# Kernel optimization log

Hardware: AMD Instinct MI355X
Metric: run time of the kernel (lower is better)

Reference implementation:

```python
import jax, jax.numpy as jnp
import numpy as np

DIM = 128
DIM_HEAD = 32
HEADS = DIM // DIM_HEAD
W1, W2, W3 = 7, 7, 7


def _rel_pos_indices():
    # matches the torch buffer construction
    g = np.stack(np.meshgrid(np.arange(W1), np.arange(W2), np.arange(W3), indexing='ij'))
    grid = g.reshape(3, -1).T  # (n, 3)
    rel = grid[:, None, :] - grid[None, :, :]
    rel[..., 0] += W1 - 1
    rel[..., 1] += W2 - 1
    rel[..., 2] += W3 - 1
    strides = np.array([(2 * W2 - 1) * (2 * W3 - 1), 2 * W3 - 1, 1])
    return (rel * strides).sum(-1).astype(np.int32)  # (n, n)


def setup_inputs() -> dict:
    key = jax.random.key(0)
    k1, k2, k3, k4 = jax.random.split(key, 4)
    x = jax.random.normal(k1, (1, 8, 8, 8, W1, W2, W3, DIM), dtype=jnp.float32)
    w_qkv = jax.random.normal(k2, (DIM, 3 * DIM), dtype=jnp.float32) * (DIM ** -0.5)
    w_out = jax.random.normal(k3, (DIM, DIM), dtype=jnp.float32) * (DIM ** -0.5)
    n_rel = (2 * W1 - 1) * (2 * W2 - 1) * (2 * W3 - 1)  # 2197
    bias_table = jax.random.normal(k4, (n_rel, HEADS), dtype=jnp.float32) * 0.02
    rel_idx = jnp.asarray(_rel_pos_indices())
    return {"x": x, "w_qkv": w_qkv, "w_out": w_out, "bias_table": bias_table, "rel_idx": rel_idx}


def reference(x, w_qkv, w_out, bias_table, rel_idx):
    b, X, Y, Z, w1, w2, w3, d = x.shape
    n = w1 * w2 * w3
    scale = DIM_HEAD ** -0.5
    xr = x.reshape(-1, n, d)                           # (B, n, d), B = b*X*Y*Z
    qkv = xr @ w_qkv                                    # (B, n, 3d)
    q, k, v = jnp.split(qkv, 3, axis=-1)
    def heads(t):
        B = t.shape[0]
        return t.reshape(B, n, HEADS, DIM_HEAD).transpose(0, 2, 1, 3)  # (B, h, n, dh)
    q, k, v = heads(q) * scale, heads(k), heads(v)
    sim = jnp.einsum('bhid,bhjd->bhij', q, k)           # (B, h, n, n)
    bias = bias_table[rel_idx]                          # (n, n, h)
    sim = sim + bias.transpose(2, 0, 1)[None]
    attn = jax.nn.softmax(sim, axis=-1)
    out = jnp.einsum('bhij,bhjd->bhid', attn, v)        # (B, h, n, dh)
    out = out.transpose(0, 2, 1, 3).reshape(-1, n, d)   # (B, n, d)
    out = out @ w_out
    return out.reshape(b, X, Y, Z, w1, w2, w3, d)
```

## Files before the change

kernel.cpp:

```cpp
#include <hip/hip_runtime.h>

#define N 343
#define NP 352
#define DIM 128
#define HEADS 4
#define DH 32

typedef float  f32x16 __attribute__((ext_vector_type(16)));
typedef float  float4v __attribute__((ext_vector_type(4)));
typedef short  short8 __attribute__((ext_vector_type(8)));
typedef unsigned uint4v __attribute__((ext_vector_type(4)));
typedef unsigned uint2v __attribute__((ext_vector_type(2)));

#define MFMA __builtin_amdgcn_mfma_f32_32x32x16_bf16

static __device__ __forceinline__ unsigned cvtpk_bf16(float lo, float hi) {
  unsigned r;
  asm("v_cvt_pk_bf16_f32 %0, %1, %2" : "=v"(r) : "v"(lo), "v"(hi));
  return r;
}
static __device__ __forceinline__ void swap32(unsigned &a, unsigned &b) {
  asm("v_permlane32_swap_b32 %0, %1" : "+v"(a), "+v"(b));
}
static __device__ __forceinline__ float exp2v(float x) {
  float r;
  asm("v_exp_f32 %0, %1" : "=v"(r) : "v"(x));
  return r;
}
static __device__ __forceinline__ float max3v(float a, float b, float c) {
  float r;
  asm("v_max3_f32 %0, %1, %2, %3" : "=v"(r) : "v"(a), "v"(b), "v"(c));
  return r;
}
static __device__ __forceinline__ unsigned short bf16u(float a) {
  unsigned u = __builtin_bit_cast(unsigned, a);
  unsigned r = u + 0x7fffu + ((u >> 16) & 1u);
  return (unsigned short)(r >> 16);
}

__global__ __launch_bounds__(256) void bias_kernel(
    const float* __restrict__ table, const int* __restrict__ rel,
    float* __restrict__ prep) {
  int row = blockIdx.x * 256 + threadIdx.x;
  if (row >= HEADS * 11 * 2 * NP) return;
  int i = row % NP;
  int t = row / NP;
  int half = t & 1;
  int tj = t >> 1;
  int jt = tj % 11;
  int h = tj / 11;
  float* dst = prep + (size_t)row * 16;
#pragma unroll
  for (int r = 0; r < 16; ++r) {
    int j = jt * 32 + (r & 3) + ((r >> 2) << 3) + (half << 2);
    float v;
    if (j >= N) v = -1.44e30f;
    else if (i >= N) v = 0.f;
    else v = table[rel[i * N + j] * HEADS + h] * 1.4426950408889634f;
    dst[r] = v;
  }
}

static __device__ __forceinline__ void attend(
    int i0, uint4v qAu, uint4v qBu,
    const unsigned short* __restrict__ Kb, const unsigned short* __restrict__ Vt,
    const float* __restrict__ bp, float* __restrict__ outw,
    int l31, int half, int swz) {
  short8 q0 = __builtin_bit_cast(short8, qAu);
  short8 q1 = __builtin_bit_cast(short8, qBu);
  const float* bpi = bp + (size_t)(i0 + l31) * 16;

  f32x16 O;
#pragma unroll
  for (int r = 0; r < 16; ++r) O[r] = 0.f;
  float m_run = -3.0e38f, l_run = 0.f;

  f32x16 Tn = *(const f32x16*)(bpi);
  for (int jt = 0; jt < 11; ++jt) {
    f32x16 T = Tn;
    if (jt < 10) Tn = *(const f32x16*)(bpi + (size_t)(jt + 1) * 11264);

    const int krow = (jt * 32 + l31) * 40;
    short8 ka0 = *(const short8*)&Kb[krow + ((half * 8) ^ swz)];
    short8 ka1 = *(const short8*)&Kb[krow + ((half * 8 + 16) ^ swz)];
    T = MFMA(ka0, q0, T, 0, 0, 0);
    T = MFMA(ka1, q1, T, 0, 0, 0);

    float g0 = max3v(T[0],  T[1],  T[2]);
    float g1 = max3v(T[3],  T[4],  T[5]);
    float g2 = max3v(T[6],  T[7],  T[8]);
    float g3 = max3v(T[9],  T[10], T[11]);
    float g4 = max3v(T[12], T[13], T[14]);
    float h0 = max3v(g0, g1, g2);
    float h1 = max3v(g3, g4, T[15]);
    float pm = fmaxf(h0, h1);
    pm = fmaxf(pm, __shfl_xor(pm, 32, 64));

    if (__any(pm > m_run + 11.5f)) {
      float nm = fmaxf(m_run, pm);
      float f = exp2v(m_run - nm);
      l_run *= f;
      m_run = nm;
#pragma unroll
      for (int r = 0; r < 16; ++r) {
        int iD = (r & 3) + ((r >> 2) << 3) + (half << 2);
        O[r] *= __shfl(f, iD, 64);
      }
    }

    float p[16];
#pragma unroll
    for (int r = 0; r < 16; ++r) p[r] = exp2v(T[r] - m_run);
    float s0 = (p[0] + p[1]) + (p[2] + p[3]);
    float s1 = (p[4] + p[5]) + (p[6] + p[7]);
    float s2 = (p[8] + p[9]) + (p[10] + p[11]);
    float s3 = (p[12] + p[13]) + (p[14] + p[15]);
    float ps = (s0 + s1) + (s2 + s3);
    l_run += ps + __shfl_xor(ps, 32, 64);

    unsigned k0 = cvtpk_bf16(p[0], p[1]),   k1 = cvtpk_bf16(p[2], p[3]);
    unsigned k2 = cvtpk_bf16(p[4], p[5]),   k3 = cvtpk_bf16(p[6], p[7]);
    unsigned k4 = cvtpk_bf16(p[8], p[9]),   k5 = cvtpk_bf16(p[10], p[11]);
    unsigned k6 = cvtpk_bf16(p[12], p[13]), k7 = cvtpk_bf16(p[14], p[15]);
    swap32(k0, k2); swap32(k1, k3); swap32(k4, k6); swap32(k5, k7);
    uint4v u1 = {k0, k1, k2, k3};
    uint4v u2 = {k4, k5, k6, k7};
    short8 pa1 = __builtin_bit_cast(short8, u1);
    short8 pa2 = __builtin_bit_cast(short8, u2);

    const int vrow = l31 * 360 + jt * 32;
    short8 vb1 = *(const short8*)&Vt[vrow + ((half * 8) ^ swz)];
    short8 vb2 = *(const short8*)&Vt[vrow + ((half * 8 + 16) ^ swz)];
    O = MFMA(pa1, vb1, O, 0, 0, 0);
    O = MFMA(pa2, vb2, O, 0, 0, 0);
  }

  float inv = 1.0f / l_run;
#pragma unroll
  for (int r = 0; r < 16; ++r) {
    int iD = (r & 3) + ((r >> 2) << 3) + (half << 2);
    float invr = __shfl(inv, iD, 64);
    int i = i0 + iD;
    if (i < N) outw[(size_t)i * DIM + l31] = O[r] * invr;
  }
}

__global__ __launch_bounds__(768, 3) void attn_kernel(
    const float* __restrict__ x, const float* __restrict__ wqkv,
    const float* __restrict__ prep, float* __restrict__ out) {
  const int b = blockIdx.x;
  const int sw = (b & 7) * ((int)gridDim.x >> 3) + (b >> 3);
  const int h = sw & 3;
  const int w = sw >> 2;
  const int tid = threadIdx.x;
  const int lane = tid & 63;
  const int wv = tid >> 6;
  const int l31 = lane & 31;
  const int half = lane >> 5;

  __shared__ __align__(16) unsigned short lds[29952];
  unsigned short* Xb0 = lds;
  unsigned short* Xb1 = lds + 8448;
  unsigned short* Wf  = lds + 16896;
  unsigned short* Kb = lds;
  unsigned short* Vt = lds + 14080;

  const float* xw = x + (size_t)w * (N * DIM);
  const int xsw = ((l31 >> 3) & 1) << 3;
  const bool act = (wv < 11);

  const int xrow0 = tid >> 2,  xg0 = (tid & 3) << 2;
  const int idx1  = tid + 768;
  const int xrow1 = idx1 >> 2, xg1 = (idx1 & 3) << 2;
  const bool hasx1 = (idx1 < 1408);
  const int xgs0 = xg0 ^ (((xrow0 >> 3) & 1) << 3);
  const int xgs1 = xg1 ^ (((xrow1 >> 3) & 1) << 3);

  float4v xr0v = {0.f, 0.f, 0.f, 0.f}, xr1v = {0.f, 0.f, 0.f, 0.f};

#define LOAD_STAGE(kc_)                                                     \
  {                                                                         \
    xr0v = *(const float4v*)(xw + xrow0 * DIM + (kc_) * 16 + xg0);          \
    xr1v[0] = 0.f; xr1v[1] = 0.f; xr1v[2] = 0.f; xr1v[3] = 0.f;             \
    if (hasx1 && xrow1 < N)                                                 \
      xr1v = *(const float4v*)(xw + xrow1 * DIM + (kc_) * 16 + xg1);        \
  }

#define WRITE_STAGE(XB_)                                                    \
  {                                                                         \
    unsigned h0_, h1_;                                                      \
    h0_ = cvtpk_bf16(xr0v[0], xr0v[1]);                                     \
    h1_ = cvtpk_bf16(xr0v[2], xr0v[3]);                                     \
    uint2v hv_ = {h0_, h1_};                                                \
    *(uint2v*)&(XB_)[xrow0 * 24 + xgs0] = hv_;                              \
    if (hasx1) {                                                            \
      h0_ = cvtpk_bf16(xr1v[0], xr1v[1]);                                   \
      h1_ = cvtpk_bf16(xr1v[2], xr1v[3]);                                   \
      uint2v hv2_ = {h0_, h1_};                                             \
      *(uint2v*)&(XB_)[xrow1 * 24 + xgs1] = hv2_;                           \
    }                                                                       \
  }

  f32x16 aQ, aK, aV;
#pragma unroll
  for (int r = 0; r < 16; ++r) { aQ[r] = 0.f; aK[r] = 0.f; aV[r] = 0.f; }

  LOAD_STAGE(0);
#pragma unroll
  for (int p = 0; p < 4; ++p) {
    int idx = tid + p * 768;
    int c = idx % 96, kg = (idx / 96) << 2;
    int col = ((c >> 5) << 7) + h * DH + (c & 31);
    const float* wp = wqkv + (size_t)kg * 384 + col;
#pragma unroll
    for (int u = 0; u < 4; ++u)
      Wf[c * 136 + kg + u] = bf16u(wp[(size_t)u * 384]);
  }

  for (int kc = 0; kc < 8; ++kc) {
    unsigned short* cur = (kc & 1) ? Xb1 : Xb0;
    WRITE_STAGE(cur);
    if (kc < 7) LOAD_STAGE(kc + 1);
    __syncthreads();

    if (act) {
      const int fo = (half * 8) ^ xsw;
      const int wfo = kc * 16 + half * 8;
      short8 xh = *(const short8*)&cur[(wv * 32 + l31) * 24 + fo];
      {
        short8 wh8 = *(const short8*)&Wf[l31 * 136 + wfo];
        aQ = MFMA(wh8, xh, aQ, 0, 0, 0);
      }
      {
        short8 wh8 = *(const short8*)&Wf[(32 + l31) * 136 + wfo];
        aK = MFMA(xh, wh8, aK, 0, 0, 0);
      }
      {
        short8 wh8 = *(const short8*)&Wf[(64 + l31) * 136 + wfo];
        aV = MFMA(xh, wh8, aV, 0, 0, 0);
      }
    }
  }

  __syncthreads();

  const float QS = 0.17677669529663687f * 1.4426950408889634f;
  uint4v qA = {0, 0, 0, 0}, qB = {0, 0, 0, 0};
  const int swz = ((l31 >> 3) & 3) << 3;
  if (act) {
    unsigned g0 = cvtpk_bf16(aQ[0] * QS, aQ[1] * QS);
    unsigned g1 = cvtpk_bf16(aQ[2] * QS, aQ[3] * QS);
    unsigned g2 = cvtpk_bf16(aQ[4] * QS, aQ[5] * QS);
    unsigned g3 = cvtpk_bf16(aQ[6] * QS, aQ[7] * QS);
    unsigned g4 = cvtpk_bf16(aQ[8] * QS, aQ[9] * QS);
    unsigned g5 = cvtpk_bf16(aQ[10] * QS, aQ[11] * QS);
    unsigned g6 = cvtpk_bf16(aQ[12] * QS, aQ[13] * QS);
    unsigned g7 = cvtpk_bf16(aQ[14] * QS, aQ[15] * QS);
    swap32(g0, g2); swap32(g1, g3); swap32(g4, g6); swap32(g5, g7);
    qA[0] = g0; qA[1] = g1; qA[2] = g2; qA[3] = g3;
    qB[0] = g4; qB[1] = g5; qB[2] = g6; qB[3] = g7;

#pragma unroll
    for (int r = 0; r < 16; ++r) {
      int iD = (r & 3) + ((r >> 2) << 3) + (half << 2);
      int cs = l31 ^ ((r >> 2) << 3);
      Kb[(wv * 32 + iD) * 40 + cs] = bf16u(aK[r]);
    }
#pragma unroll
    for (int r = 0; r < 16; r += 2) {
      int j0 = (r & 3) + ((r >> 2) << 3) + (half << 2);
      *(unsigned*)&Vt[l31 * 360 + wv * 32 + (j0 ^ swz)] =
          cvtpk_bf16(aV[r], aV[r + 1]);
    }
  }
  __syncthreads();

  if (act) {
    const float* bp = prep + ((size_t)(h * 22 + half) * NP) * 16;
    float* outw = out + (size_t)w * N * DIM + h * DH;
    attend(wv * 32, qA, qB, Kb, Vt, bp, outw, l31, half, swz);
  }
}

__global__ __launch_bounds__(768, 3) void proj_kernel(
    const float* __restrict__ wout, float* __restrict__ out) {
  const int w = blockIdx.x;
  const int tid = threadIdx.x;
  const int lane = tid & 63, wv = tid >> 6, l31 = lane & 31, half = lane >> 5;
  __shared__ __align__(16) unsigned short lds[19200];
  unsigned short* Oh = lds;
  unsigned short* W2h = lds + 14080;
  float* ow = out + (size_t)w * N * DIM;
  const int swz = ((l31 >> 3) & 3) << 3;
  const bool act = (wv < 11);

  f32x16 acc[4];
#pragma unroll
  for (int s = 0; s < 4; ++s)
#pragma unroll
    for (int r = 0; r < 16; ++r) acc[s][r] = 0.f;

  for (int kc = 0; kc < 4; ++kc) {
    __syncthreads();
#pragma unroll
    for (int p = 0; p < 4; ++p) {
      int idx = tid + p * 768;
      if (idx < 2816) {
        int row = idx >> 3, g = (idx & 7) << 2;
        float4v v = {0.f, 0.f, 0.f, 0.f};
        if (row < N) v = *(const float4v*)(ow + row * DIM + kc * 32 + g);
        unsigned h0 = cvtpk_bf16(v[0], v[1]);
        unsigned h1 = cvtpk_bf16(v[2], v[3]);
        uint2v hv = {h0, h1};
        int gs = g ^ (((row >> 3) & 3) << 3);
        *(uint2v*)&Oh[row * 40 + gs] = hv;
      }
    }
#pragma unroll
    for (int p = 0; p < 2; ++p) {
      int idx = tid + p * 768;
      if (idx < 1024) {
        int k = idx >> 5, n4 = (idx & 31) << 2;
        float4v v = *(const float4v*)(wout + (size_t)(kc * 32 + k) * DIM + n4);
#pragma unroll
        for (int u = 0; u < 4; ++u) {
          int n = n4 + u;
          int ks = k ^ (((n >> 3) & 3) << 3);
          W2h[n * 40 + ks] = bf16u(v[u]);
        }
      }
    }
    __syncthreads();
    if (act) {
#pragma unroll
      for (int kk = 0; kk < 2; ++kk) {
        int ro = (kk * 16 + half * 8) ^ swz;
        int rb = (wv * 32 + l31) * 40 + ro;
        short8 ah = *(const short8*)&Oh[rb];
#pragma unroll
        for (int s = 0; s < 4; ++s) {
          short8 bh = *(const short8*)&W2h[(s * 32 + l31) * 40 + ro];
          acc[s] = MFMA(ah, bh, acc[s], 0, 0, 0);
        }
      }
    }
  }
  if (act) {
#pragma unroll
    for (int s = 0; s < 4; ++s) {
#pragma unroll
      for (int r = 0; r < 16; ++r) {
        int iD = (r & 3) + ((r >> 2) << 3) + (half << 2);
        int i = wv * 32 + iD;
        if (i < N) ow[(size_t)i * DIM + s * 32 + l31] = acc[s][r];
      }
    }
  }
}

extern "C" void kernel_launch(void* const* d_in, const int* in_sizes, int n_in,
                              void* d_out, int out_size, void* d_ws, size_t ws_size,
                              hipStream_t stream) {
  const float* x     = (const float*)d_in[0];
  const float* wqkv  = (const float*)d_in[1];
  const float* wout  = (const float*)d_in[2];
  const float* table = (const float*)d_in[3];
  const int*   rel   = (const int*)d_in[4];
  float* out  = (float*)d_out;
  float* prep = (float*)d_ws;

  const int B = in_sizes[0] / (N * DIM);
  const int rows = HEADS * 11 * 2 * NP;

  bias_kernel<<<(rows + 255) / 256, 256, 0, stream>>>(table, rel, prep);
  attn_kernel<<<HEADS * B, 768, 0, stream>>>(x, wqkv, prep, out);
  proj_kernel<<<B, 768, 0, stream>>>(wout, out);
}
```

Measured before the change: 166.6 us.

## Halve attention block size and give each wave two query tiles

The attention kernel now launches 384 threads (6 waves) per block instead of 768 (12, one idle). Five waves each handle two 32-row query tiles and one handles a single tile, so QKV projection MFMAs reuse the loaded W fragments across both tiles and attend runs twice per wave. The cross-half row-sum shuffle is moved out of the inner loop to a single reduction at the end. This removes the idle wave and cuts per-block thread count, but serialises work within waves and raises register pressure, which may reduce occupancy or leave waves load-imbalanced.

After: 196.1 us. +17.8%, slower.

```diff
diff --git a/kernel.cpp b/kernel.cpp
--- a/kernel.cpp
+++ b/kernel.cpp
@@ -115,8 +115,7 @@
     float s1 = (p[4] + p[5]) + (p[6] + p[7]);
     float s2 = (p[8] + p[9]) + (p[10] + p[11]);
     float s3 = (p[12] + p[13]) + (p[14] + p[15]);
-    float ps = (s0 + s1) + (s2 + s3);
-    l_run += ps + __shfl_xor(ps, 32, 64);
+    l_run += (s0 + s1) + (s2 + s3);
 
     unsigned k0 = cvtpk_bf16(p[0], p[1]),   k1 = cvtpk_bf16(p[2], p[3]);
     unsigned k2 = cvtpk_bf16(p[4], p[5]),   k3 = cvtpk_bf16(p[6], p[7]);
@@ -135,6 +134,7 @@
     O = MFMA(pa2, vb2, O, 0, 0, 0);
   }
 
+  l_run += __shfl_xor(l_run, 32, 64);
   float inv = 1.0f / l_run;
 #pragma unroll
   for (int r = 0; r < 16; ++r) {
@@ -145,7 +145,7 @@
   }
 }
 
-__global__ __launch_bounds__(768, 3) void attn_kernel(
+__global__ __launch_bounds__(384, 3) void attn_kernel(
     const float* __restrict__ x, const float* __restrict__ wqkv,
     const float* __restrict__ prep, float* __restrict__ out) {
   const int b = blockIdx.x;
@@ -167,48 +167,58 @@
 
   const float* xw = x + (size_t)w * (N * DIM);
   const int xsw = ((l31 >> 3) & 1) << 3;
-  const bool act = (wv < 11);
-
-  const int xrow0 = tid >> 2,  xg0 = (tid & 3) << 2;
-  const int idx1  = tid + 768;
-  const int xrow1 = idx1 >> 2, xg1 = (idx1 & 3) << 2;
-  const bool hasx1 = (idx1 < 1408);
-  const int xgs0 = xg0 ^ (((xrow0 >> 3) & 1) << 3);
-  const int xgs1 = xg1 ^ (((xrow1 >> 3) & 1) << 3);
-
-  float4v xr0v = {0.f, 0.f, 0.f, 0.f}, xr1v = {0.f, 0.f, 0.f, 0.f};
+  const int mt0 = wv;
+  const bool two = (wv < 5);
+  const int mt1 = two ? wv + 6 : 5;
+
+  const int xrowA = tid >> 2,          xgA = (tid & 3) << 2;
+  const int xrowB = (tid + 384) >> 2,  xgB = ((tid + 384) & 3) << 2;
+  const int xrowC = (tid + 768) >> 2,  xgC = ((tid + 768) & 3) << 2;
+  const int xrowD = (tid + 1152) >> 2, xgD = ((tid + 1152) & 3) << 2;
+  const bool hasD = (tid < 256);
+  const int xgsA = xgA ^ (((xrowA >> 3) & 1) << 3);
+  const int xgsB = xgB ^ (((xrowB >> 3) & 1) << 3);
+  const int xgsC = xgC ^ (((xrowC >> 3) & 1) << 3);
+  const int xgsD = xgD ^ (((xrowD >> 3) & 1) << 3);
+
+  float4v xrA = {0.f, 0.f, 0.f, 0.f}, xrB = {0.f, 0.f, 0.f, 0.f};
+  float4v xrC = {0.f, 0.f, 0.f, 0.f}, xrD = {0.f, 0.f, 0.f, 0.f};
 
 #define LOAD_STAGE(kc_)                                                     \
   {                                                                         \
-    xr0v = *(const float4v*)(xw + xrow0 * DIM + (kc_) * 16 + xg0);          \
-    xr1v[0] = 0.f; xr1v[1] = 0.f; xr1v[2] = 0.f; xr1v[3] = 0.f;             \
-    if (hasx1 && xrow1 < N)                                                 \
-      xr1v = *(const float4v*)(xw + xrow1 * DIM + (kc_) * 16 + xg1);        \
+    xrA = *(const float4v*)(xw + xrowA * DIM + (kc_) * 16 + xgA);           \
+    xrB = *(const float4v*)(xw + xrowB * DIM + (kc_) * 16 + xgB);           \
+    xrC = *(const float4v*)(xw + xrowC * DIM + (kc_) * 16 + xgC);           \
+    xrD[0] = 0.f; xrD[1] = 0.f; xrD[2] = 0.f; xrD[3] = 0.f;                 \
+    if (hasD && xrowD < N)                                                  \
+      xrD = *(const float4v*)(xw + xrowD * DIM + (kc_) * 16 + xgD);         \
   }
 
 #define WRITE_STAGE(XB_)                                                    \
   {                                                                         \
-    unsigned h0_, h1_;                                                      \
-    h0_ = cvtpk_bf16(xr0v[0], xr0v[1]);                                     \
-    h1_ = cvtpk_bf16(xr0v[2], xr0v[3]);                                     \
-    uint2v hv_ = {h0_, h1_};                                                \
-    *(uint2v*)&(XB_)[xrow0 * 24 + xgs0] = hv_;                              \
-    if (hasx1) {                                                            \
-      h0_ = cvtpk_bf16(xr1v[0], xr1v[1]);                                   \
-      h1_ = cvtpk_bf16(xr1v[2], xr1v[3]);                                   \
-      uint2v hv2_ = {h0_, h1_};                                             \
-      *(uint2v*)&(XB_)[xrow1 * 24 + xgs1] = hv2_;                           \
+    uint2v v0 = {cvtpk_bf16(xrA[0], xrA[1]), cvtpk_bf16(xrA[2], xrA[3])};   \
+    uint2v v1 = {cvtpk_bf16(xrB[0], xrB[1]), cvtpk_bf16(xrB[2], xrB[3])};   \
+    uint2v v2 = {cvtpk_bf16(xrC[0], xrC[1]), cvtpk_bf16(xrC[2], xrC[3])};   \
+    *(uint2v*)&(XB_)[xrowA * 24 + xgsA] = v0;                               \
+    *(uint2v*)&(XB_)[xrowB * 24 + xgsB] = v1;                               \
+    *(uint2v*)&(XB_)[xrowC * 24 + xgsC] = v2;                               \
+    if (hasD) {                                                             \
+      uint2v v3 = {cvtpk_bf16(xrD[0], xrD[1]), cvtpk_bf16(xrD[2], xrD[3])}; \
+      *(uint2v*)&(XB_)[xrowD * 24 + xgsD] = v3;                             \
     }                                                                       \
   }
 
-  f32x16 aQ, aK, aV;
-#pragma unroll
-  for (int r = 0; r < 16; ++r) { aQ[r] = 0.f; aK[r] = 0.f; aV[r] = 0.f; }
+  f32x16 aQ0, aK0, aV0, aQ1, aK1, aV1;
+#pragma unroll
+  for (int r = 0; r < 16; ++r) {
+    aQ0[r] = 0.f; aK0[r] = 0.f; aV0[r] = 0.f;
+    aQ1[r] = 0.f; aK1[r] = 0.f; aV1[r] = 0.f;
+  }
 
   LOAD_STAGE(0);
 #pragma unroll
-  for (int p = 0; p < 4; ++p) {
-    int idx = tid + p * 768;
+  for (int p = 0; p < 8; ++p) {
+    int idx = tid + p * 384;
     int c = idx % 96, kg = (idx / 96) << 2;
     int col = ((c >> 5) << 7) + h * DH + (c & 31);
     const float* wp = wqkv + (size_t)kg * 384 + col;
@@ -223,63 +233,83 @@
     if (kc < 7) LOAD_STAGE(kc + 1);
     __syncthreads();
 
-    if (act) {
-      const int fo = (half * 8) ^ xsw;
-      const int wfo = kc * 16 + half * 8;
-      short8 xh = *(const short8*)&cur[(wv * 32 + l31) * 24 + fo];
-      {
-        short8 wh8 = *(const short8*)&Wf[l31 * 136 + wfo];
-        aQ = MFMA(wh8, xh, aQ, 0, 0, 0);
-      }
-      {
-        short8 wh8 = *(const short8*)&Wf[(32 + l31) * 136 + wfo];
-        aK = MFMA(xh, wh8, aK, 0, 0, 0);
-      }
-      {
-        short8 wh8 = *(const short8*)&Wf[(64 + l31) * 136 + wfo];
-        aV = MFMA(xh, wh8, aV, 0, 0, 0);
-      }
+    const int fo = (half * 8) ^ xsw;
+    const int wfo = kc * 16 + half * 8;
+    short8 xh0 = *(const short8*)&cur[(mt0 * 32 + l31) * 24 + fo];
+    short8 xh1 = xh0;
+    if (two) xh1 = *(const short8*)&cur[(mt1 * 32 + l31) * 24 + fo];
+    {
+      short8 wh8 = *(const short8*)&Wf[l31 * 136 + wfo];
+      aQ0 = MFMA(wh8, xh0, aQ0, 0, 0, 0);
+      if (two) aQ1 = MFMA(wh8, xh1, aQ1, 0, 0, 0);
+    }
+    {
+      short8 wh8 = *(const short8*)&Wf[(32 + l31) * 136 + wfo];
+      aK0 = MFMA(xh0, wh8, aK0, 0, 0, 0);
+      if (two) aK1 = MFMA(xh1, wh8, aK1, 0, 0, 0);
+    }
+    {
+      short8 wh8 = *(const short8*)&Wf[(64 + l31) * 136 + wfo];
+      aV0 = MFMA(xh0, wh8, aV0, 0, 0, 0);
+      if (two) aV1 = MFMA(xh1, wh8, aV1, 0, 0, 0);
     }
   }
 
   __syncthreads();
 
   const float QS = 0.17677669529663687f * 1.4426950408889634f;
-  uint4v qA = {0, 0, 0, 0}, qB = {0, 0, 0, 0};
+  uint4v qA0 = {0, 0, 0, 0}, qB0 = {0, 0, 0, 0};
+  uint4v qA1 = {0, 0, 0, 0}, qB1 = {0, 0, 0, 0};
   const int swz = ((l31 >> 3) & 3) << 3;
-  if (act) {
-    unsigned g0 = cvtpk_bf16(aQ[0] * QS, aQ[1] * QS);
-    unsigned g1 = cvtpk_bf16(aQ[2] * QS, aQ[3] * QS);
-    unsigned g2 = cvtpk_bf16(aQ[4] * QS, aQ[5] * QS);
-    unsigned g3 = cvtpk_bf16(aQ[6] * QS, aQ[7] * QS);
-    unsigned g4 = cvtpk_bf16(aQ[8] * QS, aQ[9] * QS);
-    unsigned g5 = cvtpk_bf16(aQ[10] * QS, aQ[11] * QS);
-    unsigned g6 = cvtpk_bf16(aQ[12] * QS, aQ[13] * QS);
-    unsigned g7 = cvtpk_bf16(aQ[14] * QS, aQ[15] * QS);
+  {
+    unsigned g0 = cvtpk_bf16(aQ0[0] * QS, aQ0[1] * QS);
+    unsigned g1 = cvtpk_bf16(aQ0[2] * QS, aQ0[3] * QS);
+    unsigned g2 = cvtpk_bf16(aQ0[4] * QS, aQ0[5] * QS);
+    unsigned g3 = cvtpk_bf16(aQ0[6] * QS, aQ0[7] * QS);
+    unsigned g4 = cvtpk_bf16(aQ0[8] * QS, aQ0[9] * QS);
+    unsigned g5 = cvtpk_bf16(aQ0[10] * QS, aQ0[11] * QS);
+    unsigned g6 = cvtpk_bf16(aQ0[12] * QS, aQ0[13] * QS);
+    unsigned g7 = cvtpk_bf16(aQ0[14] * QS, aQ0[15] * QS);
     swap32(g0, g2); swap32(g1, g3); swap32(g4, g6); swap32(g5, g7);
-    qA[0] = g0; qA[1] = g1; qA[2] = g2; qA[3] = g3;
-    qB[0] = g4; qB[1] = g5; qB[2] = g6; qB[3] = g7;
-
-#pragma unroll
-    for (int r = 0; r < 16; ++r) {
-      int iD = (r & 3) + ((r >> 2) << 3) + (half << 2);
-      int cs = l31 ^ ((r >> 2) << 3);
-      Kb[(wv * 32 + iD) * 40 + cs] = bf16u(aK[r]);
-    }
-#pragma unroll
-    for (int r = 0; r < 16; r += 2) {
-      int j0 = (r & 3) + ((r >> 2) << 3) + (half << 2);
-      *(unsigned*)&Vt[l31 * 360 + wv * 32 + (j0 ^ swz)] =
-          cvtpk_bf16(aV[r], aV[r + 1]);
-    }
+    qA0[0] = g0; qA0[1] = g1; qA0[2] = g2; qA0[3] = g3;
+    qB0[0] = g4; qB0[1] = g5; qB0[2] = g6; qB0[3] = g7;
+  }
+  if (two) {
+    unsigned g0 = cvtpk_bf16(aQ1[0] * QS, aQ1[1] * QS);
+    unsigned g1 = cvtpk_bf16(aQ1[2] * QS, aQ1[3] * QS);
+    unsigned g2 = cvtpk_bf16(aQ1[4] * QS, aQ1[5] * QS);
+    unsigned g3 = cvtpk_bf16(aQ1[6] * QS, aQ1[7] * QS);
+    unsigned g4 = cvtpk_bf16(aQ1[8] * QS, aQ1[9] * QS);
+    unsigned g5 = cvtpk_bf16(aQ1[10] * QS, aQ1[11] * QS);
+    unsigned g6 = cvtpk_bf16(aQ1[12] * QS, aQ1[13] * QS);
+    unsigned g7 = cvtpk_bf16(aQ1[14] * QS, aQ1[15] * QS);
+    swap32(g0, g2); swap32(g1, g3); swap32(g4, g6); swap32(g5, g7);
+    qA1[0] = g0; qA1[1] = g1; qA1[2] = g2; qA1[3] = g3;
+    qB1[0] = g4; qB1[1] = g5; qB1[2] = g6; qB1[3] = g7;
+  }
+
+#pragma unroll
+  for (int r = 0; r < 16; ++r) {
+    int iD = (r & 3) + ((r >> 2) << 3) + (half << 2);
+    int cs = l31 ^ ((r >> 2) << 3);
+    Kb[(mt0 * 32 + iD) * 40 + cs] = bf16u(aK0[r]);
+    if (two) Kb[(mt1 * 32 + iD) * 40 + cs] = bf16u(aK1[r]);
+  }
+#pragma unroll
+  for (int r = 0; r < 16; r += 2) {
+    int j0 = (r & 3) + ((r >> 2) << 3) + (half << 2);
+    *(unsigned*)&Vt[l31 * 360 + mt0 * 32 + (j0 ^ swz)] =
+        cvtpk_bf16(aV0[r], aV0[r + 1]);
+    if (two)
+      *(unsigned*)&Vt[l31 * 360 + mt1 * 32 + (j0 ^ swz)] =
+          cvtpk_bf16(aV1[r], aV1[r + 1]);
   }
   __syncthreads();
 
-  if (act) {
-    const float* bp = prep + ((size_t)(h * 22 + half) * NP) * 16;
-    float* outw = out + (size_t)w * N * DIM + h * DH;
-    attend(wv * 32, qA, qB, Kb, Vt, bp, outw, l31, half, swz);
-  }
+  const float* bp = prep + ((size_t)(h * 22 + half) * NP) * 16;
+  float* outw = out + (size_t)w * N * DIM + h * DH;
+  attend(mt0 * 32, qA0, qB0, Kb, Vt, bp, outw, l31, half, swz);
+  if (two) attend(mt1 * 32, qA1, qB1, Kb, Vt, bp, outw, l31, half, swz);
 }
 
 __global__ __launch_bounds__(768, 3) void proj_kernel(
@@ -373,6 +403,6 @@
   const int rows = HEADS * 11 * 2 * NP;
 
   bias_kernel<<<(rows + 255) / 256, 256, 0, stream>>>(table, rel, prep);
-  attn_kernel<<<HEADS * B, 768, 0, stream>>>(x, wqkv, prep, out);
+  attn_kernel<<<HEADS * B, 384, 0, stream>>>(x, wqkv, prep, out);
   proj_kernel<<<B, 768, 0, stream>>>(wout, out);
 }
```
